# Kernel optimization log

Hardware: AMD Instinct MI355X
Metric: run time of the kernel (lower is better)

## Reference

```python
import jax, jax.numpy as jnp
import numpy as np
import math

H = 32          # num heads
D_NOPE = 128
D_ROPE = 64
D_QK = D_NOPE + D_ROPE   # 192
D_V = 128
KV_LORA = 512
EPS = 1e-6
ROPE_THETA = 10000.0
FACTOR = 40.0
BETA_FAST, BETA_SLOW = 32.0, 1.0
ORIG_MAX_POS = 4096
MSCALE_ALL_DIM = 1.0


def _yarn_inv_freq():
    dim = D_ROPE
    pos_freqs = ROPE_THETA ** (np.arange(0, dim, 2, dtype=np.float64) / dim)
    inv_extra = 1.0 / pos_freqs
    inv_inter = 1.0 / (FACTOR * pos_freqs)

    def corr_dim(n_rot):
        return dim * math.log(ORIG_MAX_POS / (n_rot * 2 * math.pi)) / (2 * math.log(ROPE_THETA))
    low = max(math.floor(corr_dim(BETA_FAST)), 0)
    high = min(math.ceil(corr_dim(BETA_SLOW)), dim - 1)
    ramp = np.clip((np.arange(dim // 2, dtype=np.float64) - low) / max(high - low, 1e-3), 0, 1)
    inv_freq_mask = 1.0 - ramp  # extrapolation_factor = 1
    inv_freq = inv_inter * (1 - inv_freq_mask) + inv_extra * inv_freq_mask
    return jnp.asarray(inv_freq, dtype=jnp.float32)  # [D_ROPE//2]


def _apply_rope_gptj(x, cos, sin):
    # x: [T, n, D_ROPE]; cos/sin: [T, D_ROPE//2]; interleaved (is_neox_style=False)
    x2 = x.reshape(*x.shape[:-1], D_ROPE // 2, 2)
    x1, xo = x2[..., 0], x2[..., 1]
    c = cos[:, None, :]
    s = sin[:, None, :]
    r1 = x1 * c - xo * s
    r2 = xo * c + x1 * s
    return jnp.stack([r1, r2], axis=-1).reshape(x.shape)


def _rmsnorm(x, w):
    var = jnp.mean(x.astype(jnp.float32) ** 2, axis=-1, keepdims=True)
    return (x * jax.lax.rsqrt(var + EPS)) * w


def setup_inputs() -> dict:
    key = jax.random.key(0)
    ks = jax.random.split(key, 8)
    T, HID = 2048, 4096
    def w(k, shape, fan_in):
        return jax.random.normal(k, shape, dtype=jnp.float32) * (1.0 / math.sqrt(fan_in))
    return {
        "positions": jnp.arange(T, dtype=jnp.int32),
        "hidden_states": jax.random.normal(ks[0], (T, HID), dtype=jnp.float32),
        "Wqa": w(ks[1], (HID, 1536), HID),
        "q_a_ln": jnp.ones((1536,), dtype=jnp.float32),
        "Wqb": w(ks[2], (1536, H * D_QK), 1536),
        "Wkva": w(ks[3], (HID, KV_LORA + D_ROPE), HID),
        "kv_a_ln": jnp.ones((KV_LORA,), dtype=jnp.float32),
        "Wkvb": w(ks[4], (KV_LORA, H * (D_NOPE + D_V)), KV_LORA),
        "Wo": w(ks[5], (H * D_V, HID), H * D_V),
    }


def reference(positions, hidden_states, Wqa, q_a_ln, Wqb, Wkva, kv_a_ln, Wkvb, Wo):
    T = hidden_states.shape[0]
    # softmax scaling with yarn mscale correction
    mscale = 0.1 * MSCALE_ALL_DIM * math.log(FACTOR) + 1.0
    scaling = (D_QK ** -0.5) * mscale * mscale

    # --- low-rank Q path ---
    q = hidden_states @ Wqa                       # [T, 1536]
    q = _rmsnorm(q, q_a_ln)
    q = (q @ Wqb).reshape(T, H, D_QK)             # [T, H, 192]
    q_nope, q_pe = q[..., :D_NOPE], q[..., D_NOPE:]

    # --- low-rank latent KV path ---
    latent = hidden_states @ Wkva                 # [T, 576]
    kv_a = _rmsnorm(latent[:, :KV_LORA], kv_a_ln) # [T, 512]
    k_pe = latent[:, None, KV_LORA:]              # [T, 1, 64]
    kv = (kv_a @ Wkvb).reshape(T, H, D_NOPE + D_V)
    k_nope = kv[..., :D_NOPE]                     # [T, H, 128]
    v = kv[..., D_NOPE:]                          # [T, H, 128]

    # --- decoupled RoPE on rope slice only ---
    inv_freq = _yarn_inv_freq()
    freqs = positions.astype(jnp.float32)[:, None] * inv_freq[None, :]  # [T, 32]
    cos, sin = jnp.cos(freqs), jnp.sin(freqs)
    q_pe = _apply_rope_gptj(q_pe, cos, sin)       # [T, H, 64]
    k_pe = _apply_rope_gptj(k_pe, cos, sin)       # [T, 1, 64]

    q = jnp.concatenate([q_nope, q_pe], axis=-1)                      # [T, H, 192]
    k = jnp.concatenate([k_nope, jnp.broadcast_to(k_pe, (T, H, D_ROPE))], axis=-1)

    # --- causal MHA over assembled K/V ---
    scores = jnp.einsum('thd,shd->hts', q, k) * scaling               # [H, T, T]
    causal = positions[None, :, None] >= positions[None, None, :]
    scores = jnp.where(causal, scores, jnp.finfo(scores.dtype).min)
    probs = jax.nn.softmax(scores, axis=-1)
    attn = jnp.einsum('hts,shd->thd', probs, v).reshape(T, H * D_V)
    return attn @ Wo                                                   # [T, 4096]
```

## Files before the change

kernel.cpp:

```cpp
#include <hip/hip_runtime.h>
#include <math.h>

typedef __bf16 bf16x8 __attribute__((ext_vector_type(8)));
typedef float f32x4 __attribute__((ext_vector_type(4)));
typedef unsigned short u16;
typedef unsigned int u32;

#define T_SEQ 2048
#define NHEAD 32

__device__ __forceinline__ u16 f2bu(float f){
  u32 u = __float_as_uint(f);
  u32 r = (u + 0x7fffu + ((u >> 16) & 1u)) >> 16;
  return (u16)r;
}

__device__ __forceinline__ void gload_lds16(const void* g, void* l){
  __builtin_amdgcn_global_load_lds((const __attribute__((address_space(1))) u32*)g,
                                   (__attribute__((address_space(3))) u32*)l, 16, 0, 0);
}

__global__ void cast_f32_bf16(const float* __restrict__ in, u16* __restrict__ out, int n4){
  int i = blockIdx.x * blockDim.x + threadIdx.x;
  int stride = gridDim.x * blockDim.x;
  for (; i < n4; i += stride){
    float4 v = ((const float4*)in)[i];
    ushort4 o;
    o.x = f2bu(v.x); o.y = f2bu(v.y); o.z = f2bu(v.z); o.w = f2bu(v.w);
    ((ushort4*)out)[i] = o;
  }
}

__device__ __forceinline__ void tc_body(const float* __restrict__ src, u16* __restrict__ dst,
                                        int K, int N, int k0, int n0){
  __shared__ float tile[64][65];
  int t = threadIdx.x;
  int rr = t >> 4, c4 = (t & 15) * 4;
  #pragma unroll
  for (int i = 0; i < 4; i++){
    int r = rr + i * 16;
    int n = n0 + c4;
    float4 v;
    if (n < N) v = *(const float4*)(src + (size_t)(k0 + r) * N + n);
    else       v = make_float4(0.f, 0.f, 0.f, 0.f);
    tile[r][c4]     = v.x;
    tile[r][c4 + 1] = v.y;
    tile[r][c4 + 2] = v.z;
    tile[r][c4 + 3] = v.w;
  }
  __syncthreads();
  #pragma unroll
  for (int i = 0; i < 4; i++){
    int n = rr + i * 16;
    ushort4 o;
    o.x = f2bu(tile[c4 + 0][n]);
    o.y = f2bu(tile[c4 + 1][n]);
    o.z = f2bu(tile[c4 + 2][n]);
    o.w = f2bu(tile[c4 + 3][n]);
    *(ushort4*)(dst + (size_t)(n0 + n) * K + k0 + c4) = o;
  }
}

__global__ __launch_bounds__(256) void transpose_batch(
    const float* __restrict__ Wqa, u16* __restrict__ WqaT,
    const float* __restrict__ Wkva, u16* __restrict__ WkvaT,
    const float* __restrict__ Wqb, u16* __restrict__ WqbT,
    const float* __restrict__ Wkvb, u16* __restrict__ WkvbT,
    const float* __restrict__ Wo, u16* __restrict__ WoT){
  int bid = blockIdx.x;
  const float* s; u16* d; int K, N, gx, l;
  if (bid < 1536)      { s = Wqa;  d = WqaT;  K = 4096; N = 1536; gx = 64; l = bid; }
  else if (bid < 2176) { s = Wkva; d = WkvaT; K = 4096; N = 576;  gx = 64; l = bid - 1536; }
  else if (bid < 4480) { s = Wqb;  d = WqbT;  K = 1536; N = 6144; gx = 24; l = bid - 2176; }
  else if (bid < 5504) { s = Wkvb; d = WkvbT; K = 512;  N = 8192; gx = 8;  l = bid - 4480; }
  else                 { s = Wo;   d = WoT;   K = 4096; N = 4096; gx = 64; l = bid - 5504; }
  tc_body(s, d, K, N, (l % gx) * 64, (l / gx) * 64);
}

__global__ void rope_table(const int* __restrict__ positions, float* __restrict__ cosT,
                           float* __restrict__ sinT, float lo, float denom){
  int idx = blockIdx.x * blockDim.x + threadIdx.x;
  if (idx >= T_SEQ * 32) return;
  int t = idx >> 5, i = idx & 31;
  float pf = powf(10000.f, (float)i / 32.f);
  float inv_extra = 1.f / pf;
  float inv_inter = 1.f / (40.f * pf);
  float ramp = fminf(fmaxf(((float)i - lo) / denom, 0.f), 1.f);
  float invf = inv_inter * ramp + inv_extra * (1.f - ramp);
  float fr = (float)positions[t] * invf;
  cosT[idx] = cosf(fr);
  sinT[idx] = sinf(fr);
}

__global__ void rmsnorm_cast(const float* __restrict__ in, int istride, int n,
                             const float* __restrict__ w, u16* __restrict__ out, int ostride){
  int row = blockIdx.x;
  const float* x = in + (size_t)row * istride;
  float ss = 0.f;
  for (int c = threadIdx.x; c < n; c += blockDim.x){ float v = x[c]; ss += v * v; }
  #pragma unroll
  for (int off = 1; off < 64; off <<= 1) ss += __shfl_xor(ss, off);
  __shared__ float wsum[4];
  if ((threadIdx.x & 63) == 0) wsum[threadIdx.x >> 6] = ss;
  __syncthreads();
  float tot = wsum[0] + wsum[1] + wsum[2] + wsum[3];
  float scale = rsqrtf(tot / (float)n + 1e-6f);
  for (int c = threadIdx.x; c < n; c += blockDim.x)
    out[(size_t)row * ostride + c] = f2bu(x[c] * scale * w[c]);
}

__global__ void rope_kpe(const float* __restrict__ lat, int lstride, int loff,
                         const float* __restrict__ cosT,
                         const float* __restrict__ sinT, u16* __restrict__ kpe){
  int idx = blockIdx.x * blockDim.x + threadIdx.x;
  if (idx >= T_SEQ * 32) return;
  int t = idx >> 5, i = idx & 31;
  float x1 = lat[(size_t)t * lstride + loff + 2 * i];
  float x2 = lat[(size_t)t * lstride + loff + 2 * i + 1];
  float c = cosT[idx], s = sinT[idx];
  kpe[t * 64 + 2 * i]     = f2bu(x1 * c - x2 * s);
  kpe[t * 64 + 2 * i + 1] = f2bu(x2 * c + x1 * s);
}

template<int EPI>
__global__ __launch_bounds__(256) void gemm_bt(const u16* __restrict__ A, const u16* __restrict__ BT,
                                               float* __restrict__ C, u16* __restrict__ O1,
                                               u16* __restrict__ O2,
                                               const float* __restrict__ cosT,
                                               const float* __restrict__ sinT,
                                               float scaling, int M, int N, int K){
  __shared__ __align__(1024) char lds[32768];
  const int tid = threadIdx.x;
  const int wave = tid >> 6, lane = tid & 63;
  const int lg = lane >> 4, lm = lane & 15;

  int gx = gridDim.x;
  int nwg = gx * gridDim.y;
  int orig = blockIdx.y * gx + blockIdx.x;
  int qq = nwg >> 3, rr_ = nwg & 7, xc = orig & 7, rest = orig >> 3;
  int wg = (xc < rr_ ? xc * (qq + 1) : rr_ * (qq + 1) + (xc - rr_) * qq) + rest;
  const int bn = (wg % gx) * 128, bm = (wg / gx) * 128;

  const int wr = (wave >> 1) * 64, wc = (wave & 1) * 64;
  f32x4 acc[4][4] = {};
  int srow[2], scol[2], soff[2];
  #pragma unroll
  for (int j = 0; j < 2; j++){
    int o = (wave * 2 + j) * 1024 + lane * 16;
    int row = o >> 6;
    int cg = ((o >> 4) & 3) ^ ((row >> 1) & 3);
    srow[j] = row; scol[j] = cg * 8; soff[j] = (wave * 2 + j) * 1024;
  }

  #pragma unroll
  for (int j = 0; j < 2; j++){
    gload_lds16(A  + (size_t)(bm + srow[j]) * K + scol[j], lds + soff[j]);
    gload_lds16(BT + (size_t)(bn + srow[j]) * K + scol[j], lds + 16384 + soff[j]);
  }

  int cur = 0;
  for (int k0 = 0; k0 < K; k0 += 32){
    if (k0 + 32 < K){
      char* dA = lds + (cur ^ 1) * 8192;
      char* dB = lds + 16384 + (cur ^ 1) * 8192;
      #pragma unroll
      for (int j = 0; j < 2; j++){
        gload_lds16(A  + (size_t)(bm + srow[j]) * K + k0 + 32 + scol[j], dA + soff[j]);
        gload_lds16(BT + (size_t)(bn + srow[j]) * K + k0 + 32 + scol[j], dB + soff[j]);
      }
      asm volatile("s_waitcnt vmcnt(4)" ::: "memory");
    } else {
      asm volatile("s_waitcnt vmcnt(0)" ::: "memory");
    }
    __builtin_amdgcn_sched_barrier(0);
    __builtin_amdgcn_s_barrier();

    const char* ldsA = lds + cur * 8192;
    const char* ldsB = lds + 16384 + cur * 8192;
    bf16x8 af[4], bfr[4];
    #pragma unroll
    for (int m = 0; m < 4; m++){
      int r = wr + m * 16 + lm;
      af[m] = *(const bf16x8*)(ldsA + r * 64 + ((lg ^ ((r >> 1) & 3)) << 4));
    }
    #pragma unroll
    for (int n = 0; n < 4; n++){
      int r = wc + n * 16 + lm;
      bfr[n] = *(const bf16x8*)(ldsB + r * 64 + ((lg ^ ((r >> 1) & 3)) << 4));
    }
    __builtin_amdgcn_s_setprio(1);
    #pragma unroll
    for (int m = 0; m < 4; m++)
      #pragma unroll
      for (int n = 0; n < 4; n++)
        acc[m][n] = __builtin_amdgcn_mfma_f32_16x16x32_bf16(af[m], bfr[n], acc[m][n], 0, 0, 0);
    __builtin_amdgcn_s_setprio(0);
    __builtin_amdgcn_s_barrier();
    cur ^= 1;
  }

  #pragma unroll
  for (int m = 0; m < 4; m++)
    #pragma unroll
    for (int n = 0; n < 4; n++){
      const int r0 = bm + wr + m * 16 + lg * 4;
      const int c  = bn + wc + n * 16 + lm;
      if (EPI == 0){
        #pragma unroll
        for (int q = 0; q < 4; q++)
          C[(size_t)(r0 + q) * N + c] = acc[m][n][q];
      } else if (EPI == 1){
        #pragma unroll
        for (int q = 0; q < 4; q++){
          float v = acc[m][n][q];
          float vp = __shfl_xor(v, 1);
          int h = c / 192, d = c - h * 192;
          float outv;
          if (d < 128) outv = v;
          else {
            int i = (d - 128) >> 1;
            float co = cosT[(r0 + q) * 32 + i], si = sinT[(r0 + q) * 32 + i];
            outv = (d & 1) ? (v * co + vp * si) : (v * co - vp * si);
          }
          O1[(size_t)h * T_SEQ * 192 + (size_t)(r0 + q) * 192 + d] = f2bu(outv * scaling);
        }
      } else {
        int h = c >> 8, d = c & 255;
        if (d < 128){
          #pragma unroll
          for (int q = 0; q < 4; q++)
            O1[(size_t)h * T_SEQ * 128 + (size_t)(r0 + q) * 128 + d] = f2bu(acc[m][n][q]);
        } else {
          ushort4 o;
          o.x = f2bu(acc[m][n][0]); o.y = f2bu(acc[m][n][1]);
          o.z = f2bu(acc[m][n][2]); o.w = f2bu(acc[m][n][3]);
          *(ushort4*)(O2 + (size_t)(h * 128 + (d - 128)) * T_SEQ + r0) = o;
        }
      }
    }
}

__global__ __launch_bounds__(512, 4) void flash_attn(const u16* __restrict__ Qp, const u16* __restrict__ Kp,
                                                     const u16* __restrict__ kpe, const u16* __restrict__ Vt,
                                                     u16* __restrict__ attnb){
  const int b = blockIdx.x;
  const int h = (b & 7) + 8 * ((b >> 3) & 3);
  const int qt = (b < 256) ? (15 - (b >> 5)) : ((b - 256) >> 5);
  const int tid = threadIdx.x;
  const int wave = tid >> 6, lane = tid & 63;
  const int lg = lane >> 4, lm = lane & 15;
  const int qbase = qt * 128 + wave * 16;

  __shared__ __align__(1024) char lds[51200];
  u16* Pw = (u16*)(lds + 40960 + wave * 1280);

  const u16* KpH = Kp + (size_t)h * T_SEQ * 128;
  const u16* VtH = Vt + (size_t)h * 128 * T_SEQ;

  int kO[2], kLoc[2], kPE[2];
  #pragma unroll
  for (int j = 0; j < 2; j++){
    int o = tid + 512 * j;
    int r = (o / 24) & 31, c = o % 24;
    int cx = c ^ (r & 7);
    kO[j] = o * 16;
    if (cx < 16){ kPE[j] = 0; kLoc[j] = r * 128 + cx * 8; }
    else        { kPE[j] = 1; kLoc[j] = r * 64 + (cx - 16) * 8; }
  }
  int vO, vSrc;
  { int o = tid; int d = o >> 2, c = o & 3; vO = o * 16; vSrc = d * T_SEQ + ((c ^ ((d >> 1) & 3)) << 3); }

  #define STAGE_KV(t, bi)                                                              \
    do {                                                                               \
      char* _k = lds + (bi) * 12288;                                                   \
      char* _v = lds + 24576 + (bi) * 8192;                                            \
      { const u16* _s = kPE[0] ? (kpe + (size_t)(t) * 2048 + kLoc[0])                  \
                               : (KpH + (size_t)(t) * 4096 + kLoc[0]);                 \
        gload_lds16(_s, _k + kO[0]); }                                                 \
      if (tid < 256){                                                                  \
        const u16* _s = kPE[1] ? (kpe + (size_t)(t) * 2048 + kLoc[1])                  \
                               : (KpH + (size_t)(t) * 4096 + kLoc[1]);                 \
        gload_lds16(_s, _k + kO[1]); }                                                 \
      gload_lds16(VtH + vSrc + (t) * 32, _v + vO);                                     \
    } while (0)

  const int nt = 4 * qt + 4;

  bf16x8 qf[6];
  const u16* Qbase = Qp + (size_t)(h * T_SEQ + qbase + lm) * 192 + lg * 8;
  #pragma unroll
  for (int dk = 0; dk < 6; dk++) qf[dk] = *(const bf16x8*)(Qbase + dk * 32);

  f32x4 o_[8] = {};
  float m_[4], l_[4];
  #pragma unroll
  for (int q = 0; q < 4; q++){ m_[q] = -3.0e38f; l_[q] = 0.f; }

  STAGE_KV(0, 0);

  #pragma unroll 1
  for (int kt = 0; kt < nt; kt++){
    const int t0 = kt * 32;
    const int bsel = kt & 1;
    asm volatile("s_waitcnt vmcnt(0)" ::: "memory");
    __builtin_amdgcn_sched_barrier(0);
    __builtin_amdgcn_s_barrier();
    if (kt + 1 < nt) STAGE_KV(kt + 1, bsel ^ 1);
    const char* Kb = lds + bsel * 12288;
    const char* Vb = lds + 24576 + bsel * 8192;

    f32x4 s_[2] = {};
    __builtin_amdgcn_s_setprio(1);
    #pragma unroll
    for (int hh = 0; hh < 2; hh++){
      const int r = hh * 16 + lm;
      const int rb = r * 384, rx = r & 7;
      #pragma unroll
      for (int dk = 0; dk < 6; dk++){
        bf16x8 kf = *(const bf16x8*)(Kb + rb + (((dk * 4 + lg) ^ rx) << 4));
        s_[hh] = __builtin_amdgcn_mfma_f32_16x16x32_bf16(qf[dk], kf, s_[hh], 0, 0, 0);
      }
    }
    __builtin_amdgcn_s_setprio(0);
    #pragma unroll
    for (int hh = 0; hh < 2; hh++)
      #pragma unroll
      for (int q = 0; q < 4; q++){
        int col = t0 + hh * 16 + lm;
        int qrow = qbase + lg * 4 + q;
        if (col > qrow) s_[hh][q] = -3.0e38f;
      }
    float pm[4];
    #pragma unroll
    for (int q = 0; q < 4; q++) pm[q] = fmaxf(s_[0][q], s_[1][q]);
    int ok = (pm[0] <= m_[0] + 8.f) & (pm[1] <= m_[1] + 8.f) &
             (pm[2] <= m_[2] + 8.f) & (pm[3] <= m_[3] + 8.f);
    if (!__all(ok)){
      #pragma unroll
      for (int q = 0; q < 4; q++){
        float v = pm[q];
        #pragma unroll
        for (int off = 8; off; off >>= 1) v = fmaxf(v, __shfl_xor(v, off));
        float mn = fmaxf(m_[q], v);
        float alpha = (m_[q] <= -1.0e37f) ? 0.f : exp2f(m_[q] - mn);
        l_[q] *= alpha;
        #pragma unroll
        for (int n = 0; n < 8; n++) o_[n][q] *= alpha;
        m_[q] = mn;
      }
    }
    #pragma unroll
    for (int q = 0; q < 4; q++){
      #pragma unroll
      for (int hh = 0; hh < 2; hh++){
        float p = exp2f(s_[hh][q] - m_[q]);
        l_[q] += p;
        Pw[(lg * 4 + q) * 40 + hh * 16 + lm] = f2bu(p);
      }
    }
    asm volatile("s_waitcnt lgkmcnt(0)" ::: "memory");
    __builtin_amdgcn_sched_barrier(0);
    bf16x8 pf = *(const bf16x8*)((const char*)Pw + lm * 80 + lg * 16);
    __builtin_amdgcn_s_setprio(1);
    #pragma unroll
    for (int n = 0; n < 8; n++){
      const int d = n * 16 + lm;
      bf16x8 vf = *(const bf16x8*)(Vb + d * 64 + ((lg ^ ((d >> 1) & 3)) << 4));
      o_[n] = __builtin_amdgcn_mfma_f32_16x16x32_bf16(pf, vf, o_[n], 0, 0, 0);
    }
    __builtin_amdgcn_s_setprio(0);
  }

  #pragma unroll
  for (int q = 0; q < 4; q++){
    #pragma unroll
    for (int off = 8; off; off >>= 1) l_[q] += __shfl_xor(l_[q], off);
  }
  float inv[4];
  #pragma unroll
  for (int q = 0; q < 4; q++) inv[q] = 1.f / l_[q];
  #pragma unroll
  for (int n = 0; n < 8; n++)
    #pragma unroll
    for (int q = 0; q < 4; q++){
      int r = qbase + lg * 4 + q;
      attnb[(size_t)r * 4096 + h * 128 + n * 16 + lm] = f2bu(o_[n][q] * inv[q]);
    }
  #undef STAGE_KV
}

extern "C" void kernel_launch(void* const* d_in, const int* in_sizes, int n_in,
                              void* d_out, int out_size, void* d_ws, size_t ws_size,
                              hipStream_t stream){
  const int*   positions = (const int*)d_in[0];
  const float* hidden    = (const float*)d_in[1];
  const float* Wqa       = (const float*)d_in[2];
  const float* q_a_ln    = (const float*)d_in[3];
  const float* Wqb       = (const float*)d_in[4];
  const float* Wkva      = (const float*)d_in[5];
  const float* kv_a_ln   = (const float*)d_in[6];
  const float* Wkvb      = (const float*)d_in[7];
  const float* Wo        = (const float*)d_in[8];
  float* out = (float*)d_out;
  char* ws = (char*)d_ws;

  const size_t o_hidB  = 0;
  const size_t o_cos   = 16777216;
  const size_t o_sin   = 17039360;
  const size_t o_kpe   = 17301504;
  const size_t o_comb  = 17563648;
  const size_t o_qln   = 35389440;
  const size_t o_kva   = 41680896;
  const size_t o_WqaT  = 43778048;
  const size_t o_WkvaT = 56360960;
  const size_t o_WqbT  = 61603840;
  const size_t o_WkvbT = 80478208;
  const size_t o_Qp    = 88866816;
  const size_t o_Kp    = 114032640;
  const size_t o_Vt    = 147587072;
  const size_t o_WoT   = 164364288;

  u16*   hidB  = (u16*)(ws + o_hidB);
  u16*   attnb = (u16*)(ws + o_hidB);
  float* cosT  = (float*)(ws + o_cos);
  float* sinT  = (float*)(ws + o_sin);
  u16*   kpe   = (u16*)(ws + o_kpe);
  float* comb  = (float*)(ws + o_comb);
  u16*   qln   = (u16*)(ws + o_qln);
  u16*   kva   = (u16*)(ws + o_kva);
  u16*   WqaT  = (u16*)(ws + o_WqaT);
  u16*   WkvaT = (u16*)(ws + o_WkvaT);
  u16*   WqbT  = (u16*)(ws + o_WqbT);
  u16*   WkvbT = (u16*)(ws + o_WkvbT);
  u16*   Qp    = (u16*)(ws + o_Qp);
  u16*   Kp    = (u16*)(ws + o_Kp);
  u16*   Vt    = (u16*)(ws + o_Vt);
  u16*   WoT   = (u16*)(ws + o_WoT);

  double mscale = 0.1 * log(40.0) + 1.0;
  double scaling_d = pow(192.0, -0.5) * mscale * mscale;
  float scaling_log2 = (float)(scaling_d * 1.4426950408889634);
  const double PI = 3.14159265358979323846;
  double cd_fast = 64.0 * log(4096.0 / (32.0 * 2.0 * PI)) / (2.0 * log(10000.0));
  double cd_slow = 64.0 * log(4096.0 / ( 1.0 * 2.0 * PI)) / (2.0 * log(10000.0));
  double lo_d = fmax(floor(cd_fast), 0.0);
  double hi_d = fmin(ceil(cd_slow), 63.0);
  float lo = (float)lo_d;
  float denom = (float)fmax(hi_d - lo_d, 0.001);

  transpose_batch<<<9600, 256, 0, stream>>>(Wqa, WqaT, Wkva, WkvaT, Wqb, WqbT,
                                            Wkvb, WkvbT, Wo, WoT);
  cast_f32_bf16<<<2048, 256, 0, stream>>>(hidden, hidB, T_SEQ * 4096 / 4);
  rope_table<<<256, 256, 0, stream>>>(positions, cosT, sinT, lo, denom);
  gemm_bt<0><<<dim3(2176 / 128, 2048 / 128), 256, 0, stream>>>(hidB, WqaT, comb, nullptr, nullptr,
                                                               nullptr, nullptr, 0.f, 2048, 2176, 4096);
  rmsnorm_cast<<<2048, 256, 0, stream>>>(comb, 2176, 1536, q_a_ln, qln, 1536);
  rmsnorm_cast<<<2048, 256, 0, stream>>>(comb + 1536, 2176, 512, kv_a_ln, kva, 512);
  rope_kpe<<<256, 256, 0, stream>>>(comb, 2176, 2048, cosT, sinT, kpe);
  gemm_bt<1><<<dim3(6144 / 128, 2048 / 128), 256, 0, stream>>>(qln, WqbT, nullptr, Qp, nullptr,
                                                               cosT, sinT, scaling_log2, 2048, 6144, 1536);
  gemm_bt<2><<<dim3(8192 / 128, 2048 / 128), 256, 0, stream>>>(kva, WkvbT, nullptr, Kp, Vt,
                                                               nullptr, nullptr, 0.f, 2048, 8192, 512);
  flash_attn<<<512, 512, 0, stream>>>(Qp, Kp, kpe, Vt, attnb);
  gemm_bt<0><<<dim3(4096 / 128, 2048 / 128), 256, 0, stream>>>(attnb, WoT, out, nullptr, nullptr,
                                                               nullptr, nullptr, 0.f, 2048, 4096, 4096);
}
```

Before: 397.4 us.

## Process two 16-row query groups per wave in flash attention

The flash attention block drops from 8 waves to 4, and each wave now handles 32 query rows as two 16-row groups. Each K and V fragment read from LDS is reused for two MFMAs, which halves LDS read traffic per unit of compute. Staging loads are spread over the 256 threads with three K and two V loads each. In exchange, register pressure roughly doubles for Q fragments, accumulators and softmax state, and fewer waves are resident to hide latency; launch bounds change to (256,2).

New measurement: 410.3 us. 3.2% more time.

```diff
diff --git a/kernel.cpp b/kernel.cpp
--- a/kernel.cpp
+++ b/kernel.cpp
@@ -240,7 +240,7 @@
     }
 }
 
-__global__ __launch_bounds__(512, 4) void flash_attn(const u16* __restrict__ Qp, const u16* __restrict__ Kp,
+__global__ __launch_bounds__(256, 2) void flash_attn(const u16* __restrict__ Qp, const u16* __restrict__ Kp,
                                                      const u16* __restrict__ kpe, const u16* __restrict__ Vt,
                                                      u16* __restrict__ attnb){
   const int b = blockIdx.x;
@@ -249,52 +249,62 @@
   const int tid = threadIdx.x;
   const int wave = tid >> 6, lane = tid & 63;
   const int lg = lane >> 4, lm = lane & 15;
-  const int qbase = qt * 128 + wave * 16;
+  const int qbase = qt * 128 + wave * 32;
 
   __shared__ __align__(1024) char lds[51200];
-  u16* Pw = (u16*)(lds + 40960 + wave * 1280);
+  u16* Pw = (u16*)(lds + 40960 + wave * 2560);
 
   const u16* KpH = Kp + (size_t)h * T_SEQ * 128;
   const u16* VtH = Vt + (size_t)h * 128 * T_SEQ;
 
-  int kO[2], kLoc[2], kPE[2];
-  #pragma unroll
-  for (int j = 0; j < 2; j++){
-    int o = tid + 512 * j;
-    int r = (o / 24) & 31, c = o % 24;
+  int kO[3], kLoc[3], kPE[3];
+  #pragma unroll
+  for (int j = 0; j < 3; j++){
+    int o = tid + 256 * j;
+    int r = o / 24, c = o - (o / 24) * 24;
     int cx = c ^ (r & 7);
     kO[j] = o * 16;
     if (cx < 16){ kPE[j] = 0; kLoc[j] = r * 128 + cx * 8; }
     else        { kPE[j] = 1; kLoc[j] = r * 64 + (cx - 16) * 8; }
   }
-  int vO, vSrc;
-  { int o = tid; int d = o >> 2, c = o & 3; vO = o * 16; vSrc = d * T_SEQ + ((c ^ ((d >> 1) & 3)) << 3); }
+  int vO[2], vSrc[2];
+  #pragma unroll
+  for (int j = 0; j < 2; j++){
+    int o = tid + 256 * j;
+    int d = o >> 2, c = o & 3;
+    vO[j] = o * 16; vSrc[j] = d * T_SEQ + ((c ^ ((d >> 1) & 3)) << 3);
+  }
 
   #define STAGE_KV(t, bi)                                                              \
     do {                                                                               \
       char* _k = lds + (bi) * 12288;                                                   \
       char* _v = lds + 24576 + (bi) * 8192;                                            \
-      { const u16* _s = kPE[0] ? (kpe + (size_t)(t) * 2048 + kLoc[0])                  \
-                               : (KpH + (size_t)(t) * 4096 + kLoc[0]);                 \
-        gload_lds16(_s, _k + kO[0]); }                                                 \
-      if (tid < 256){                                                                  \
-        const u16* _s = kPE[1] ? (kpe + (size_t)(t) * 2048 + kLoc[1])                  \
-                               : (KpH + (size_t)(t) * 4096 + kLoc[1]);                 \
-        gload_lds16(_s, _k + kO[1]); }                                                 \
-      gload_lds16(VtH + vSrc + (t) * 32, _v + vO);                                     \
+      _Pragma("unroll")                                                                \
+      for (int j = 0; j < 3; j++){                                                     \
+        const u16* _s = kPE[j] ? (kpe + (size_t)(t) * 2048 + kLoc[j])                  \
+                               : (KpH + (size_t)(t) * 4096 + kLoc[j]);                 \
+        gload_lds16(_s, _k + kO[j]);                                                   \
+      }                                                                                \
+      _Pragma("unroll")                                                                \
+      for (int j = 0; j < 2; j++) gload_lds16(VtH + vSrc[j] + (t) * 32, _v + vO[j]);   \
     } while (0)
 
   const int nt = 4 * qt + 4;
 
-  bf16x8 qf[6];
-  const u16* Qbase = Qp + (size_t)(h * T_SEQ + qbase + lm) * 192 + lg * 8;
-  #pragma unroll
-  for (int dk = 0; dk < 6; dk++) qf[dk] = *(const bf16x8*)(Qbase + dk * 32);
-
-  f32x4 o_[8] = {};
-  float m_[4], l_[4];
-  #pragma unroll
-  for (int q = 0; q < 4; q++){ m_[q] = -3.0e38f; l_[q] = 0.f; }
+  bf16x8 qf[2][6];
+  #pragma unroll
+  for (int g = 0; g < 2; g++){
+    const u16* Qbase = Qp + (size_t)(h * T_SEQ + qbase + g * 16 + lm) * 192 + lg * 8;
+    #pragma unroll
+    for (int dk = 0; dk < 6; dk++) qf[g][dk] = *(const bf16x8*)(Qbase + dk * 32);
+  }
+
+  f32x4 o_[2][8] = {};
+  float m_[2][4], l_[2][4];
+  #pragma unroll
+  for (int g = 0; g < 2; g++)
+    #pragma unroll
+    for (int q = 0; q < 4; q++){ m_[g][q] = -3.0e38f; l_[g][q] = 0.f; }
 
   STAGE_KV(0, 0);
 
@@ -309,7 +319,7 @@
     const char* Kb = lds + bsel * 12288;
     const char* Vb = lds + 24576 + bsel * 8192;
 
-    f32x4 s_[2] = {};
+    f32x4 s_[2][2] = {};
     __builtin_amdgcn_s_setprio(1);
     #pragma unroll
     for (int hh = 0; hh < 2; hh++){
@@ -318,74 +328,89 @@
       #pragma unroll
       for (int dk = 0; dk < 6; dk++){
         bf16x8 kf = *(const bf16x8*)(Kb + rb + (((dk * 4 + lg) ^ rx) << 4));
-        s_[hh] = __builtin_amdgcn_mfma_f32_16x16x32_bf16(qf[dk], kf, s_[hh], 0, 0, 0);
+        s_[0][hh] = __builtin_amdgcn_mfma_f32_16x16x32_bf16(qf[0][dk], kf, s_[0][hh], 0, 0, 0);
+        s_[1][hh] = __builtin_amdgcn_mfma_f32_16x16x32_bf16(qf[1][dk], kf, s_[1][hh], 0, 0, 0);
       }
     }
     __builtin_amdgcn_s_setprio(0);
     #pragma unroll
-    for (int hh = 0; hh < 2; hh++)
+    for (int g = 0; g < 2; g++)
+      #pragma unroll
+      for (int hh = 0; hh < 2; hh++)
+        #pragma unroll
+        for (int q = 0; q < 4; q++){
+          int col = t0 + hh * 16 + lm;
+          int qrow = qbase + g * 16 + lg * 4 + q;
+          if (col > qrow) s_[g][hh][q] = -3.0e38f;
+        }
+    float pm[2][4];
+    int ok = 1;
+    #pragma unroll
+    for (int g = 0; g < 2; g++)
       #pragma unroll
       for (int q = 0; q < 4; q++){
-        int col = t0 + hh * 16 + lm;
-        int qrow = qbase + lg * 4 + q;
-        if (col > qrow) s_[hh][q] = -3.0e38f;
+        pm[g][q] = fmaxf(s_[g][0][q], s_[g][1][q]);
+        ok &= (pm[g][q] <= m_[g][q] + 8.f);
       }
-    float pm[4];
-    #pragma unroll
-    for (int q = 0; q < 4; q++) pm[q] = fmaxf(s_[0][q], s_[1][q]);
-    int ok = (pm[0] <= m_[0] + 8.f) & (pm[1] <= m_[1] + 8.f) &
-             (pm[2] <= m_[2] + 8.f) & (pm[3] <= m_[3] + 8.f);
     if (!__all(ok)){
       #pragma unroll
-      for (int q = 0; q < 4; q++){
-        float v = pm[q];
+      for (int g = 0; g < 2; g++)
         #pragma unroll
-        for (int off = 8; off; off >>= 1) v = fmaxf(v, __shfl_xor(v, off));
-        float mn = fmaxf(m_[q], v);
-        float alpha = (m_[q] <= -1.0e37f) ? 0.f : exp2f(m_[q] - mn);
-        l_[q] *= alpha;
+        for (int q = 0; q < 4; q++){
+          float v = pm[g][q];
+          #pragma unroll
+          for (int off = 8; off; off >>= 1) v = fmaxf(v, __shfl_xor(v, off));
+          float mn = fmaxf(m_[g][q], v);
+          float alpha = (m_[g][q] <= -1.0e37f) ? 0.f : exp2f(m_[g][q] - mn);
+          l_[g][q] *= alpha;
+          #pragma unroll
+          for (int n = 0; n < 8; n++) o_[g][n][q] *= alpha;
+          m_[g][q] = mn;
+        }
+    }
+    #pragma unroll
+    for (int g = 0; g < 2; g++)
+      #pragma unroll
+      for (int q = 0; q < 4; q++)
         #pragma unroll
-        for (int n = 0; n < 8; n++) o_[n][q] *= alpha;
-        m_[q] = mn;
-      }
-    }
-    #pragma unroll
-    for (int q = 0; q < 4; q++){
-      #pragma unroll
-      for (int hh = 0; hh < 2; hh++){
-        float p = exp2f(s_[hh][q] - m_[q]);
-        l_[q] += p;
-        Pw[(lg * 4 + q) * 40 + hh * 16 + lm] = f2bu(p);
-      }
-    }
+        for (int hh = 0; hh < 2; hh++){
+          float p = exp2f(s_[g][hh][q] - m_[g][q]);
+          l_[g][q] += p;
+          Pw[(g * 16 + lg * 4 + q) * 40 + hh * 16 + lm] = f2bu(p);
+        }
     asm volatile("s_waitcnt lgkmcnt(0)" ::: "memory");
     __builtin_amdgcn_sched_barrier(0);
-    bf16x8 pf = *(const bf16x8*)((const char*)Pw + lm * 80 + lg * 16);
+    bf16x8 pf0 = *(const bf16x8*)((const char*)Pw + lm * 80 + lg * 16);
+    bf16x8 pf1 = *(const bf16x8*)((const char*)Pw + 1280 + lm * 80 + lg * 16);
     __builtin_amdgcn_s_setprio(1);
     #pragma unroll
     for (int n = 0; n < 8; n++){
       const int d = n * 16 + lm;
       bf16x8 vf = *(const bf16x8*)(Vb + d * 64 + ((lg ^ ((d >> 1) & 3)) << 4));
-      o_[n] = __builtin_amdgcn_mfma_f32_16x16x32_bf16(pf, vf, o_[n], 0, 0, 0);
+      o_[0][n] = __builtin_amdgcn_mfma_f32_16x16x32_bf16(pf0, vf, o_[0][n], 0, 0, 0);
+      o_[1][n] = __builtin_amdgcn_mfma_f32_16x16x32_bf16(pf1, vf, o_[1][n], 0, 0, 0);
     }
     __builtin_amdgcn_s_setprio(0);
   }
 
   #pragma unroll
-  for (int q = 0; q < 4; q++){
-    #pragma unroll
-    for (int off = 8; off; off >>= 1) l_[q] += __shfl_xor(l_[q], off);
-  }
-  float inv[4];
-  #pragma unroll
-  for (int q = 0; q < 4; q++) inv[q] = 1.f / l_[q];
-  #pragma unroll
-  for (int n = 0; n < 8; n++)
+  for (int g = 0; g < 2; g++){
     #pragma unroll
     for (int q = 0; q < 4; q++){
-      int r = qbase + lg * 4 + q;
-      attnb[(size_t)r * 4096 + h * 128 + n * 16 + lm] = f2bu(o_[n][q] * inv[q]);
-    }
+      #pragma unroll
+      for (int off = 8; off; off >>= 1) l_[g][q] += __shfl_xor(l_[g][q], off);
+    }
+    float inv[4];
+    #pragma unroll
+    for (int q = 0; q < 4; q++) inv[q] = 1.f / l_[g][q];
+    #pragma unroll
+    for (int n = 0; n < 8; n++)
+      #pragma unroll
+      for (int q = 0; q < 4; q++){
+        int r = qbase + g * 16 + lg * 4 + q;
+        attnb[(size_t)r * 4096 + h * 128 + n * 16 + lm] = f2bu(o_[g][n][q] * inv[q]);
+      }
+  }
   #undef STAGE_KV
 }
 
@@ -461,7 +486,7 @@
                                                                cosT, sinT, scaling_log2, 2048, 6144, 1536);
   gemm_bt<2><<<dim3(8192 / 128, 2048 / 128), 256, 0, stream>>>(kva, WkvbT, nullptr, Kp, Vt,
                                                                nullptr, nullptr, 0.f, 2048, 8192, 512);
-  flash_attn<<<512, 512, 0, stream>>>(Qp, Kp, kpe, Vt, attnb);
+  flash_attn<<<512, 256, 0, stream>>>(Qp, Kp, kpe, Vt, attnb);
   gemm_bt<0><<<dim3(4096 / 128, 2048 / 128), 256, 0, stream>>>(attnb, WoT, out, nullptr, nullptr,
                                                                nullptr, nullptr, 0.f, 2048, 4096, 4096);
 }
```
